# Kernel tuning notes

Hardware: AMD Instinct MI355X
Metric: run time of the kernel (lower is better)

The kernel has to match this reference:

```python
import jax, jax.numpy as jnp
import numpy as np

B, S, D, H, HD = 2, 2048, 1024, 16, 64
DFF = 4 * D
EPS = 1e-6


def _rms(x, w):
    return w * (x * jax.lax.rsqrt(jnp.mean(x * x, axis=-1, keepdims=True) + EPS))


def _rope(x, rope):
    # x: [B, H, S, HD], rope: [S, HD, 2]
    cos = rope[..., 0][None, None]
    sin = rope[..., 1][None, None]
    xr = x.reshape(*x.shape[:-1], -1, 2)
    rot = jnp.stack([-xr[..., 1], xr[..., 0]], axis=-1).reshape(x.shape)
    return x * cos + rot * sin


def setup_inputs() -> dict:
    key = jax.random.key(0)
    ks = jax.random.split(key, 10)
    w = lambda k, shape: jax.random.normal(k, shape, jnp.float32) * 0.02
    return {
        "hidden_states": jax.random.normal(ks[0], (B, S, D), jnp.float32),
        "timestep": jax.random.normal(ks[1], (B, D), jnp.float32),
        "rope_pos_embed": jax.random.normal(ks[2], (S, HD, 2), jnp.float32),
        "adaln_w": w(ks[3], (6 * D, D)),
        "adaln_b": jnp.zeros((6 * D,), jnp.float32),
        "wq": w(ks[4], (D, D)),
        "wk": w(ks[5], (D, D)),
        "wv": w(ks[6], (D, D)),
        "wo": w(ks[7], (D, D)),
        "q_norm_w": jnp.ones((D,), jnp.float32),
        "k_norm_w": jnp.ones((D,), jnp.float32),
        "norm3_w": jnp.ones((D,), jnp.float32),
        "fc1_w": w(ks[8], (DFF, D)),
        "fc1_b": jnp.zeros((DFF,), jnp.float32),
        "fc2_w": w(ks[9], (D, DFF)),
        "fc2_b": jnp.zeros((D,), jnp.float32),
    }


def reference(hidden_states, timestep, rope_pos_embed, adaln_w, adaln_b,
              wq, wk, wv, wo, q_norm_w, k_norm_w, norm3_w,
              fc1_w, fc1_b, fc2_w, fc2_b):
    x = hidden_states  # [B, S, D]
    # AdaLayerNorm: emb = Linear(SiLU(timestep)) -> 6 modulation chunks, broadcast over seq
    emb = jax.nn.silu(timestep) @ adaln_w.T + adaln_b  # [B, 6D]
    sh_msa, sc_msa, g_msa, sh_mlp, sc_mlp, g_mlp = jnp.split(emb[:, None, :], 6, axis=-1)
    mu = jnp.mean(x, axis=-1, keepdims=True)
    var = jnp.mean((x - mu) ** 2, axis=-1, keepdims=True)
    ln = (x - mu) * jax.lax.rsqrt(var + EPS)
    xm = ln * (1.0 + sc_msa) + sh_msa  # modulated input to attention

    # Attention: projections + RMSNorm over inner_dim + RoPE + SDPA
    q = _rms(xm @ wq.T, q_norm_w)
    k = _rms(xm @ wk.T, k_norm_w)
    v = xm @ wv.T
    q = q.reshape(B, S, H, HD).transpose(0, 2, 1, 3)
    k = k.reshape(B, S, H, HD).transpose(0, 2, 1, 3)
    v = v.reshape(B, S, H, HD).transpose(0, 2, 1, 3)
    q = _rope(q, rope_pos_embed)
    k = _rope(k, rope_pos_embed)
    scores = jnp.einsum('bhqd,bhkd->bhqk', q, k) * (HD ** -0.5)
    attn = jax.nn.softmax(scores, axis=-1)
    o = jnp.einsum('bhqk,bhkd->bhqd', attn, v)
    o = o.transpose(0, 2, 1, 3).reshape(B, S, H * HD) @ wo.T

    h = x + g_msa * o  # gated residual

    # MLP branch with AdaLN scale/shift on RMSNorm output
    n3 = _rms(h, norm3_w)
    nm = n3 * (1.0 + sc_mlp) + sh_mlp
    ff = jax.nn.gelu(nm @ fc1_w.T + fc1_b, approximate=True) @ fc2_w.T + fc2_b
    return h + g_mlp * ff
```

## Files before the change

### kernel.cpp

```cpp
#include <hip/hip_runtime.h>
#include <cstdint>
#include <cstddef>

typedef unsigned short ushort_t;
typedef __attribute__((ext_vector_type(8))) short s8v;
typedef __attribute__((ext_vector_type(4))) short s4v;
typedef __attribute__((ext_vector_type(4))) float f4v;

#define MFMA16(a, b, c) __builtin_amdgcn_mfma_f32_16x16x32_bf16(a, b, c, 0, 0, 0)

__device__ __forceinline__ ushort_t f2bf(float f) {
  union { float f; unsigned u; } a; a.f = f;
  return (ushort_t)((a.u + 0x7fffu + ((a.u >> 16) & 1u)) >> 16);
}
__device__ __forceinline__ float bf2f(ushort_t h) {
  union { unsigned u; float f; } a; a.u = ((unsigned)h) << 16; return a.f;
}
__device__ __forceinline__ unsigned fbits(float f) {
  union { float f; unsigned u; } a; a.f = f; return a.u;
}

__device__ __forceinline__ void gload16(const void* g, void* l) {
  __builtin_amdgcn_global_load_lds(
      (__attribute__((address_space(1))) void*)(uintptr_t)g,
      (__attribute__((address_space(3))) void*)(unsigned)(uintptr_t)l,
      16, 0, 0);
}

__launch_bounds__(256)
__global__ void convert_w(const float* __restrict__ wq, const float* __restrict__ wk,
                          const float* __restrict__ wv, const float* __restrict__ wo,
                          const float* __restrict__ f1, const float* __restrict__ f2,
                          ushort_t* __restrict__ dqkv, ushort_t* __restrict__ dwo,
                          ushort_t* __restrict__ df1, ushort_t* __restrict__ df2)
{
  const int blk = blockIdx.x;
  const float* src; ushort_t* dst; int off;
  if      (blk < 1024) { src = wq; dst = dqkv;            off = blk; }
  else if (blk < 2048) { src = wk; dst = dqkv + 1048576;  off = blk - 1024; }
  else if (blk < 3072) { src = wv; dst = dqkv + 2097152;  off = blk - 2048; }
  else if (blk < 4096) { src = wo; dst = dwo;             off = blk - 3072; }
  else if (blk < 8192) { src = f1; dst = df1;             off = blk - 4096; }
  else                 { src = f2; dst = df2;             off = blk - 8192; }
  const int idx = off * 1024 + threadIdx.x * 4;
  float4 v = *(const float4*)(src + idx);
  s4v o;
  o[0] = (short)f2bf(v.x); o[1] = (short)f2bf(v.y);
  o[2] = (short)f2bf(v.z); o[3] = (short)f2bf(v.w);
  *(s4v*)(dst + idx) = o;
}

__launch_bounds__(256)
__global__ void adaln(const float* __restrict__ ts, const float* __restrict__ w,
                      const float* __restrict__ bias, float* __restrict__ emb)
{
  const int j = blockIdx.x * 4 + (threadIdx.x >> 6);
  const int lane = threadIdx.x & 63;
  const float* wr = w + (size_t)j * 1024;
  float s0 = 0.f, s1 = 0.f;
  for (int i = lane; i < 1024; i += 64) {
    const float wv = wr[i];
    const float t0 = ts[i], t1 = ts[1024 + i];
    const float e0 = __builtin_amdgcn_exp2f(-1.4426950409f * t0);
    const float e1 = __builtin_amdgcn_exp2f(-1.4426950409f * t1);
    s0 += wv * t0 * __builtin_amdgcn_rcpf(1.f + e0);
    s1 += wv * t1 * __builtin_amdgcn_rcpf(1.f + e1);
  }
  #pragma unroll
  for (int m = 32; m; m >>= 1) { s0 += __shfl_down(s0, m); s1 += __shfl_down(s1, m); }
  if (!lane) { emb[j] = s0 + bias[j]; emb[6144 + j] = s1 + bias[j]; }
}

__launch_bounds__(256)
__global__ void ln_mod(const float* __restrict__ x, const float* __restrict__ emb,
                       ushort_t* __restrict__ xm)
{
  const int row = blockIdx.x, b = row >> 11, tid = threadIdx.x;
  const float* xr = x + (size_t)row * 1024;
  const int c = tid * 4;
  float4 v = *(const float4*)(xr + c);
  float s  = v.x + v.y + v.z + v.w;
  float s2 = v.x*v.x + v.y*v.y + v.z*v.z + v.w*v.w;
  #pragma unroll
  for (int m = 32; m; m >>= 1) { s += __shfl_down(s, m); s2 += __shfl_down(s2, m); }
  __shared__ float red[8];
  const int wave = tid >> 6, lane = tid & 63;
  if (!lane) { red[wave] = s; red[4 + wave] = s2; }
  __syncthreads();
  const float mu = (red[0] + red[1] + red[2] + red[3]) * (1.f / 1024.f);
  const float ms = (red[4] + red[5] + red[6] + red[7]) * (1.f / 1024.f);
  const float rstd = rsqrtf(ms - mu * mu + 1e-6f);
  const float* sh = emb + b * 6144;
  const float* sc = emb + b * 6144 + 1024;
  float4 shv = *(const float4*)(sh + c);
  float4 scv = *(const float4*)(sc + c);
  s4v ov;
  ov[0] = (short)f2bf((v.x - mu) * rstd * (1.f + scv.x) + shv.x);
  ov[1] = (short)f2bf((v.y - mu) * rstd * (1.f + scv.y) + shv.y);
  ov[2] = (short)f2bf((v.z - mu) * rstd * (1.f + scv.z) + shv.z);
  ov[3] = (short)f2bf((v.w - mu) * rstd * (1.f + scv.w) + shv.w);
  *(s4v*)(xm + (size_t)row * 1024 + c) = ov;
}

template<int EPI, int TN>
__launch_bounds__(256)
__global__ void gemm_bt(const ushort_t* __restrict__ A, const ushort_t* __restrict__ Bw,
                        int K, int N,
                        ushort_t* __restrict__ outb, float* __restrict__ outf,
                        const float* __restrict__ bias, const float* __restrict__ resid,
                        const float* __restrict__ emb, int gate_off)
{
  constexpr int JN = TN / 32;
  constexpr int BUFB = TN * 32;
  __shared__ ushort_t As0[128 * 32], As1[128 * 32];
  __shared__ ushort_t Bs0[BUFB],    Bs1[BUFB];
  const int tid = threadIdx.x;
  const int wave = tid >> 6, lane = tid & 63;
  const int quad = lane >> 4, r = lane & 15;
  const int m0 = blockIdx.y * 128, n0 = blockIdx.x * TN;
  const int wm = (wave >> 1) * 64, wn = (wave & 1) * (TN / 2);

  const int srow = wave * 16 + (lane >> 2);
  const int scol = (lane & 3) * 8;
  const ushort_t* ag = A  + (size_t)(m0 + srow) * K + scol;
  const ushort_t* bg = Bw + (size_t)(n0 + srow) * K + scol;
  const size_t rowK64 = (size_t)64 * K;

  f4v acc[4][JN] = {};

  auto stage = [&](ushort_t* as, ushort_t* bs) {
    gload16(ag,          as + wave * 512);
    gload16(ag + rowK64, as + wave * 512 + 2048);
    gload16(bg,          bs + wave * 512);
    if (TN == 128) gload16(bg + rowK64, bs + wave * 512 + 2048);
    ag += 32; bg += 32;
  };
  auto compute = [&](const ushort_t* ab, const ushort_t* bb) {
    s8v af[4], bf[JN];
    #pragma unroll
    for (int i = 0; i < 4; i++)
      af[i] = *(const s8v*)(ab + (wm + i * 16 + r) * 32 + quad * 8);
    #pragma unroll
    for (int j = 0; j < JN; j++)
      bf[j] = *(const s8v*)(bb + (wn + j * 16 + r) * 32 + quad * 8);
    #pragma unroll
    for (int i = 0; i < 4; i++)
      #pragma unroll
      for (int j = 0; j < JN; j++)
        acc[i][j] = MFMA16(af[i], bf[j], acc[i][j]);
  };

  stage(As0, Bs0);
  __syncthreads();
  const int R = (K >> 6) - 1;
  for (int it = 0; it < R; it++) {
    stage(As1, Bs1);
    compute(As0, Bs0);
    __syncthreads();
    stage(As0, Bs0);
    compute(As1, Bs1);
    __syncthreads();
  }
  stage(As1, Bs1);
  compute(As0, Bs0);
  __syncthreads();
  compute(As1, Bs1);

  const int bblk = m0 >> 11;
  #pragma unroll
  for (int j = 0; j < JN; j++) {
    const int col = n0 + wn + j * 16 + r;
    float bj = 0.f, gj = 0.f;
    if (EPI == 2 || EPI == 3) bj = bias[col];
    if (EPI == 1 || EPI == 3) gj = emb[bblk * 6144 + gate_off + col];
    #pragma unroll
    for (int i = 0; i < 4; i++) {
      const int row = m0 + wm + i * 16 + quad * 4;
      #pragma unroll
      for (int rr = 0; rr < 4; rr++) {
        float v = acc[i][j][rr];
        const size_t idx = (size_t)(row + rr) * N + col;
        if (EPI == 0) {
          outb[idx] = f2bf(v);
        } else if (EPI == 1) {
          outf[idx] = resid[idx] + gj * v;
        } else if (EPI == 2) {
          v += bj;
          const float t = fmaf(v * v, 0.1029436f, 2.3022083f);
          const float e = __builtin_amdgcn_exp2f(-v * t);
          outb[idx] = f2bf(v * __builtin_amdgcn_rcpf(1.f + e));
        } else {
          outf[idx] = resid[idx] + gj * (v + bj);
        }
      }
    }
  }
}

__launch_bounds__(256, 2)
__global__ void gemm256(const ushort_t* __restrict__ A, const ushort_t* __restrict__ Bw,
                        int K, int N,
                        ushort_t* __restrict__ outb, const float* __restrict__ bias)
{
  __shared__ ushort_t As0[256 * 32], As1[256 * 32];
  __shared__ ushort_t Bs0[128 * 32], Bs1[128 * 32];
  const int tid = threadIdx.x;
  const int wave = tid >> 6, lane = tid & 63;
  const int quad = lane >> 4, r = lane & 15;
  const int m0 = blockIdx.y * 256, n0 = blockIdx.x * 128;
  const int wm = (wave >> 1) * 128, wn = (wave & 1) * 64;

  const int srow = wave * 16 + (lane >> 2);
  const int scol = (lane & 3) * 8;
  const ushort_t* ag = A  + (size_t)(m0 + srow) * K + scol;
  const ushort_t* bg = Bw + (size_t)(n0 + srow) * K + scol;
  const size_t rowK64 = (size_t)64 * K;

  f4v acc[8][4] = {};

  auto stage = [&](ushort_t* as, ushort_t* bs) {
    #pragma unroll
    for (int sg = 0; sg < 4; sg++)
      gload16(ag + sg * rowK64, as + sg * 2048 + wave * 512);
    #pragma unroll
    for (int sg = 0; sg < 2; sg++)
      gload16(bg + sg * rowK64, bs + sg * 2048 + wave * 512);
    ag += 32; bg += 32;
  };
  auto compute = [&](const ushort_t* ab, const ushort_t* bb) {
    s8v bf[4];
    #pragma unroll
    for (int j = 0; j < 4; j++)
      bf[j] = *(const s8v*)(bb + (wn + j * 16 + r) * 32 + quad * 8);
    #pragma unroll
    for (int i = 0; i < 8; i++) {
      s8v af = *(const s8v*)(ab + (wm + i * 16 + r) * 32 + quad * 8);
      #pragma unroll
      for (int j = 0; j < 4; j++)
        acc[i][j] = MFMA16(af, bf[j], acc[i][j]);
    }
  };

  stage(As0, Bs0);
  __syncthreads();
  const int R = (K >> 6) - 1;
  for (int it = 0; it < R; it++) {
    stage(As1, Bs1);
    compute(As0, Bs0);
    __syncthreads();
    stage(As0, Bs0);
    compute(As1, Bs1);
    __syncthreads();
  }
  stage(As1, Bs1);
  compute(As0, Bs0);
  __syncthreads();
  compute(As1, Bs1);

  #pragma unroll
  for (int j = 0; j < 4; j++) {
    const int col = n0 + wn + j * 16 + r;
    const float bj = bias[col];
    #pragma unroll
    for (int i = 0; i < 8; i++) {
      const int row = m0 + wm + i * 16 + quad * 4;
      #pragma unroll
      for (int rr = 0; rr < 4; rr++) {
        float v = acc[i][j][rr] + bj;
        const float t = fmaf(v * v, 0.1029436f, 2.3022083f);
        const float e = __builtin_amdgcn_exp2f(-v * t);
        outb[(size_t)(row + rr) * N + col] =
            f2bf(v * __builtin_amdgcn_rcpf(1.f + e));
      }
    }
  }
}

__launch_bounds__(256)
__global__ void qkv_post(const ushort_t* __restrict__ qkv, const float* __restrict__ rope,
                         const float* __restrict__ qw, const float* __restrict__ kw,
                         ushort_t* __restrict__ q_r, ushort_t* __restrict__ k_r,
                         ushort_t* __restrict__ v_r)
{
  const int row = blockIdx.x, b = row >> 11, s = row & 2047, tid = threadIdx.x;
  const ushort_t* base = qkv + (size_t)row * 3072;
  const int c = tid * 4;
  s4v qv = *(const s4v*)(base + c);
  s4v kv = *(const s4v*)(base + 1024 + c);
  s4v vv = *(const s4v*)(base + 2048 + c);
  float qf[4], kf[4]; float sq = 0.f, sk = 0.f;
  #pragma unroll
  for (int i = 0; i < 4; i++) {
    qf[i] = bf2f((ushort_t)qv[i]); kf[i] = bf2f((ushort_t)kv[i]);
    sq += qf[i] * qf[i]; sk += kf[i] * kf[i];
  }
  #pragma unroll
  for (int m = 32; m; m >>= 1) { sq += __shfl_down(sq, m); sk += __shfl_down(sk, m); }
  __shared__ float red[8];
  const int wave = tid >> 6, lane = tid & 63;
  if (!lane) { red[wave] = sq; red[4 + wave] = sk; }
  __syncthreads();
  const float rq = rsqrtf((red[0]+red[1]+red[2]+red[3]) * (1.f/1024.f) + 1e-6f)
                   * 0.18033688011112042f;
  const float rk = rsqrtf((red[4]+red[5]+red[6]+red[7]) * (1.f/1024.f) + 1e-6f);

  const int h = c >> 6, d = c & 63;
  const float* rp = rope + ((size_t)s * 64 + d) * 2;
  float4 r01 = *(const float4*)(rp);
  float4 r23 = *(const float4*)(rp + 4);
  const float q0 = qf[0]*rq*qw[c], q1 = qf[1]*rq*qw[c+1];
  const float q2 = qf[2]*rq*qw[c+2], q3 = qf[3]*rq*qw[c+3];
  const float k0 = kf[0]*rk*kw[c], k1 = kf[1]*rk*kw[c+1];
  const float k2 = kf[2]*rk*kw[c+2], k3 = kf[3]*rk*kw[c+3];
  s4v qo, ko;
  qo[0] = (short)f2bf(q0 * r01.x - q1 * r01.y);
  qo[1] = (short)f2bf(q1 * r01.z + q0 * r01.w);
  qo[2] = (short)f2bf(q2 * r23.x - q3 * r23.y);
  qo[3] = (short)f2bf(q3 * r23.z + q2 * r23.w);
  ko[0] = (short)f2bf(k0 * r01.x - k1 * r01.y);
  ko[1] = (short)f2bf(k1 * r01.z + k0 * r01.w);
  ko[2] = (short)f2bf(k2 * r23.x - k3 * r23.y);
  ko[3] = (short)f2bf(k3 * r23.z + k2 * r23.w);
  const size_t rowbase = ((size_t)(b * 16 + h) * 2048 + s) * 64;
  const int d_s = (((d >> 3) ^ (s & 7)) << 3) | (d & 7);
  *(s4v*)(q_r + rowbase + d) = qo;
  *(s4v*)(k_r + rowbase + d_s) = ko;
  *(s4v*)(v_r + rowbase + d) = vv;
}

__launch_bounds__(256)
__global__ void vtrans(const ushort_t* __restrict__ v_r, ushort_t* __restrict__ v_t)
{
  const int bh = blockIdx.x >> 5, st = blockIdx.x & 31;
  const int s0 = st * 64;
  __shared__ ushort_t tile[64 * 72];
  const int tid = threadIdx.x;
  #pragma unroll
  for (int rep = 0; rep < 2; rep++) {
    const int idx = rep * 256 + tid;
    const int sr = idx >> 3, dc = (idx & 7) << 3;
    s8v val = *(const s8v*)(v_r + ((size_t)bh * 2048 + s0 + sr) * 64 + dc);
    *(s8v*)(tile + sr * 72 + dc) = val;
  }
  __syncthreads();
  #pragma unroll
  for (int rep = 0; rep < 2; rep++) {
    const int idx = rep * 256 + tid;
    const int d = idx >> 3;
    const int scs = (((idx & 7) ^ (d & 7)) << 3);
    s8v val;
    const int sc = (idx & 7) << 3;
    #pragma unroll
    for (int j = 0; j < 8; j++) val[j] = (short)tile[(sc + j) * 72 + d];
    *(s8v*)(v_t + ((size_t)bh * 64 + d) * 2048 + s0 + scs) = val;
  }
}

__launch_bounds__(256)
__global__ void flash(const ushort_t* __restrict__ q_r, const ushort_t* __restrict__ k_r,
                      const ushort_t* __restrict__ v_t, ushort_t* __restrict__ attn)
{
  __shared__ ushort_t Ksh[128 * 64];
  __shared__ ushort_t Vsh[64 * 128];
  __shared__ ushort_t Psh[4][16 * 128];
  const int bh = blockIdx.x >> 5, qb = blockIdx.x & 31;
  const int tid = threadIdx.x, wave = tid >> 6, lane = tid & 63;
  const int quad = lane >> 4, r = lane & 15;
  const int rx = r & 7;
  const int q0 = qb * 64 + wave * 16;
  const size_t bhS = (size_t)bh * 2048;

  s8v aq0 = *(const s8v*)(q_r + (bhS + q0 + r) * 64 + quad * 8);
  s8v aq1 = *(const s8v*)(q_r + (bhS + q0 + r) * 64 + 32 + quad * 8);

  f4v o[4] = {};
  float mi = -1e30f, li = 0.f;

  const ushort_t* kg = k_r + (bhS + wave * 32 + (lane >> 3)) * 64 + (lane & 7) * 8;
  ushort_t* kl = Ksh + wave * 2048 + lane * 8;
  const ushort_t* vg = v_t + ((size_t)bh * 64 + wave * 16 + (lane >> 4)) * 2048
                       + (lane & 15) * 8;
  ushort_t* vl = Vsh + (wave * 16 + (lane >> 4)) * 128 + (lane & 15) * 8;
  ushort_t* pw = &Psh[wave][0];

  for (int kb = 0; kb < 2048; kb += 128) {
    __syncthreads();
    #pragma unroll
    for (int c = 0; c < 4; c++) {
      gload16(kg + (size_t)(kb + c * 8) * 64, kl + c * 512);
      gload16(vg + kb + (size_t)(c * 4) * 2048, vl + c * 512);
    }
    __syncthreads();

    f4v st[8];
    #pragma unroll
    for (int t = 0; t < 8; t++) {
      const ushort_t* krow = Ksh + (t * 16 + r) * 64;
      s8v k0 = *(const s8v*)(krow + ((quad ^ rx) << 3));
      s8v k1 = *(const s8v*)(krow + (((4 + quad) ^ rx) << 3));
      f4v z = {};
      z = MFMA16(k0, aq0, z);
      z = MFMA16(k1, aq1, z);
      st[t] = z;
    }

    float m4[8];
    #pragma unroll
    for (int t = 0; t < 8; t++)
      m4[t] = fmaxf(fmaxf(st[t][0], st[t][1]), fmaxf(st[t][2], st[t][3]));
    float mloc = fmaxf(fmaxf(fmaxf(m4[0], m4[1]), fmaxf(m4[2], m4[3])),
                       fmaxf(fmaxf(m4[4], m4[5]), fmaxf(m4[6], m4[7])));
    mloc = fmaxf(mloc, __shfl_xor(mloc, 16));
    mloc = fmaxf(mloc, __shfl_xor(mloc, 32));
    const float mn = fmaxf(mi, mloc);
    const float al = __builtin_amdgcn_exp2f(mi - mn);

    float p[8][4];
    uint2 pk[8];
    #pragma unroll
    for (int t = 0; t < 8; t++) {
      #pragma unroll
      for (int rr = 0; rr < 4; rr++)
        p[t][rr] = __builtin_amdgcn_exp2f(st[t][rr] - mn);
      const unsigned u0 = fbits(p[t][0]) + 0x8000u;
      const unsigned u1 = fbits(p[t][1]) + 0x8000u;
      const unsigned u2 = fbits(p[t][2]) + 0x8000u;
      const unsigned u3 = fbits(p[t][3]) + 0x8000u;
      pk[t].x = __builtin_amdgcn_perm(u1, u0, 0x07060302u);
      pk[t].y = __builtin_amdgcn_perm(u3, u2, 0x07060302u);
    }

    #pragma unroll
    for (int t = 0; t < 8; t++) {
      const int cw = t * 2 + (quad >> 1);
      const int sc = (cw & 8) | ((cw & 7) ^ rx);
      *(uint2*)(pw + r * 128 + (sc << 3) + (quad & 1) * 4) = pk[t];
    }

    float alo[4];
    #pragma unroll
    for (int rr = 0; rr < 4; rr++) alo[rr] = __shfl(al, quad * 4 + rr);
    #pragma unroll
    for (int nt = 0; nt < 4; nt++)
      #pragma unroll
      for (int rr = 0; rr < 4; rr++) o[nt][rr] *= alo[rr];

    float s4r[8];
    #pragma unroll
    for (int t = 0; t < 8; t++)
      s4r[t] = (p[t][0] + p[t][1]) + (p[t][2] + p[t][3]);
    float ls = ((s4r[0] + s4r[1]) + (s4r[2] + s4r[3])) +
               ((s4r[4] + s4r[5]) + (s4r[6] + s4r[7]));
    ls += __shfl_xor(ls, 16);
    ls += __shfl_xor(ls, 32);
    li = al * li + ls;
    mi = mn;

    asm volatile("s_waitcnt lgkmcnt(0)" ::: "memory");

    #pragma unroll
    for (int kc = 0; kc < 4; kc++) {
      const int c = kc * 4 + quad;
      const int sc = (c & 8) | ((c & 7) ^ rx);
      s8v ap = *(const s8v*)(pw + r * 128 + (sc << 3));
      #pragma unroll
      for (int nt = 0; nt < 4; nt++) {
        s8v bv = *(const s8v*)(Vsh + (nt * 16 + r) * 128 + (sc << 3));
        o[nt] = MFMA16(ap, bv, o[nt]);
      }
    }
  }

  const int h = bh & 15, b = bh >> 4;
  const float linv = 1.f / li;
  #pragma unroll
  for (int rr = 0; rr < 4; rr++) {
    const float inv = __shfl(linv, quad * 4 + rr);
    const size_t orow = ((size_t)(b * 2048 + q0 + quad * 4 + rr)) * 1024 + h * 64;
    #pragma unroll
    for (int nt = 0; nt < 4; nt++)
      attn[orow + nt * 16 + r] = f2bf(o[nt][rr] * inv);
  }
}

__launch_bounds__(256)
__global__ void rms3_mod(const float* __restrict__ h, const float* __restrict__ emb,
                         const float* __restrict__ w3, ushort_t* __restrict__ nm)
{
  const int row = blockIdx.x, b = row >> 11, tid = threadIdx.x;
  const float* hr = h + (size_t)row * 1024;
  const int c = tid * 4;
  float4 v = *(const float4*)(hr + c);
  float s2 = v.x*v.x + v.y*v.y + v.z*v.z + v.w*v.w;
  #pragma unroll
  for (int m = 32; m; m >>= 1) s2 += __shfl_down(s2, m);
  __shared__ float red[4];
  const int wave = tid >> 6, lane = tid & 63;
  if (!lane) red[wave] = s2;
  __syncthreads();
  const float rms = rsqrtf((red[0] + red[1] + red[2] + red[3]) * (1.f / 1024.f) + 1e-6f);
  const float* sh = emb + b * 6144 + 3072;
  const float* sc = emb + b * 6144 + 4096;
  float4 shv = *(const float4*)(sh + c);
  float4 scv = *(const float4*)(sc + c);
  float4 wv  = *(const float4*)(w3 + c);
  s4v ov;
  ov[0] = (short)f2bf(v.x * rms * wv.x * (1.f + scv.x) + shv.x);
  ov[1] = (short)f2bf(v.y * rms * wv.y * (1.f + scv.y) + shv.y);
  ov[2] = (short)f2bf(v.z * rms * wv.z * (1.f + scv.z) + shv.z);
  ov[3] = (short)f2bf(v.w * rms * wv.w * (1.f + scv.w) + shv.w);
  *(s4v*)(nm + (size_t)row * 1024 + c) = ov;
}

extern "C" void kernel_launch(void* const* d_in, const int* in_sizes, int n_in,
                              void* d_out, int out_size, void* d_ws, size_t ws_size,
                              hipStream_t stream)
{
  const float* x    = (const float*)d_in[0];
  const float* ts   = (const float*)d_in[1];
  const float* rope = (const float*)d_in[2];
  const float* adw  = (const float*)d_in[3];
  const float* adb  = (const float*)d_in[4];
  const float* wq   = (const float*)d_in[5];
  const float* wk   = (const float*)d_in[6];
  const float* wv   = (const float*)d_in[7];
  const float* wo   = (const float*)d_in[8];
  const float* qnw  = (const float*)d_in[9];
  const float* knw  = (const float*)d_in[10];
  const float* n3w  = (const float*)d_in[11];
  const float* f1w  = (const float*)d_in[12];
  const float* f1b  = (const float*)d_in[13];
  const float* f2w  = (const float*)d_in[14];
  const float* f2b  = (const float*)d_in[15];

  char* ws = (char*)d_ws;
  ushort_t* WQKV = (ushort_t*)(ws + 0);
  ushort_t* WO   = (ushort_t*)(ws + 6291456);
  ushort_t* F1   = (ushort_t*)(ws + 8388608);
  ushort_t* F2   = (ushort_t*)(ws + 16777216);
  float*    EMB  = (float*)   (ws + 25165824);
  float*    H    = (float*)   (ws + 25214976);
  ushort_t* XM   = (ushort_t*)(ws + 41992192);
  ushort_t* QKV  = (ushort_t*)(ws + 50380800);
  ushort_t* QR   = (ushort_t*)(ws + 75546624);
  ushort_t* KR   = (ushort_t*)(ws + 83935232);
  ushort_t* VR   = (ushort_t*)(ws + 92323840);
  ushort_t* VT   = (ushort_t*)(ws + 100712448);
  ushort_t* ATTN = XM;
  ushort_t* NM   = QKV;
  ushort_t* FF1  = QR;

  convert_w<<<12288, 256, 0, stream>>>(wq, wk, wv, wo, f1w, f2w, WQKV, WO, F1, F2);
  adaln<<<1536, 256, 0, stream>>>(ts, adw, adb, EMB);
  ln_mod<<<4096, 256, 0, stream>>>(x, EMB, XM);
  gemm_bt<0, 128><<<dim3(24, 32), 256, 0, stream>>>(XM, WQKV, 1024, 3072,
      QKV, nullptr, nullptr, nullptr, nullptr, 0);
  qkv_post<<<4096, 256, 0, stream>>>(QKV, rope, qnw, knw, QR, KR, VR);
  vtrans<<<1024, 256, 0, stream>>>(VR, VT);
  flash<<<1024, 256, 0, stream>>>(QR, KR, VT, ATTN);
  gemm_bt<1, 64><<<dim3(16, 32), 256, 0, stream>>>(ATTN, WO, 1024, 1024,
      nullptr, H, nullptr, x, EMB, 2048);
  rms3_mod<<<4096, 256, 0, stream>>>(H, EMB, n3w, NM);
  gemm256<<<dim3(32, 16), 256, 0, stream>>>(NM, F1, 1024, 4096, FF1, f1b);
  gemm_bt<3, 64><<<dim3(16, 32), 256, 0, stream>>>(FF1, F2, 4096, 1024,
      nullptr, (float*)d_out, f2b, H, EMB, 5120);
}
```

Measured before the change: 425.7 us.

## Double-buffer K/V tiles in flash attention and raise wave priority around MFMAs

The flash attention kernel now keeps two LDS buffers for K and V. It issues the global-to-LDS loads for the next 128-key tile while the current tile is being computed, replacing the load, barrier, compute sequence with a ping-pong pipeline. It also wraps the QK and PV MFMA loops in s_setprio to favour matrix issue. The aim is to hide global load latency behind compute. In exchange, LDS per block grows from about 48KB to 80KB, which may lower occupancy.

Result: faster. 414.7 us (-2.6%).

```diff
diff --git a/kernel.cpp b/kernel.cpp
--- a/kernel.cpp
+++ b/kernel.cpp
@@ -360,8 +360,8 @@
 __global__ void flash(const ushort_t* __restrict__ q_r, const ushort_t* __restrict__ k_r,
                       const ushort_t* __restrict__ v_t, ushort_t* __restrict__ attn)
 {
-  __shared__ ushort_t Ksh[128 * 64];
-  __shared__ ushort_t Vsh[64 * 128];
+  __shared__ ushort_t Ksh[2][128 * 64];
+  __shared__ ushort_t Vsh[2][64 * 128];
   __shared__ ushort_t Psh[4][16 * 128];
   const int bh = blockIdx.x >> 5, qb = blockIdx.x & 31;
   const int tid = threadIdx.x, wave = tid >> 6, lane = tid & 63;
@@ -377,25 +377,26 @@
   float mi = -1e30f, li = 0.f;
 
   const ushort_t* kg = k_r + (bhS + wave * 32 + (lane >> 3)) * 64 + (lane & 7) * 8;
-  ushort_t* kl = Ksh + wave * 2048 + lane * 8;
   const ushort_t* vg = v_t + ((size_t)bh * 64 + wave * 16 + (lane >> 4)) * 2048
                        + (lane & 15) * 8;
-  ushort_t* vl = Vsh + (wave * 16 + (lane >> 4)) * 128 + (lane & 15) * 8;
+  const int klo = wave * 2048 + lane * 8;
+  const int vlo = (wave * 16 + (lane >> 4)) * 128 + (lane & 15) * 8;
   ushort_t* pw = &Psh[wave][0];
 
-  for (int kb = 0; kb < 2048; kb += 128) {
-    __syncthreads();
+  auto stage = [&](ushort_t* kbuf, ushort_t* vbuf, int kb) {
     #pragma unroll
     for (int c = 0; c < 4; c++) {
-      gload16(kg + (size_t)(kb + c * 8) * 64, kl + c * 512);
-      gload16(vg + kb + (size_t)(c * 4) * 2048, vl + c * 512);
-    }
-    __syncthreads();
-
+      gload16(kg + (size_t)(kb + c * 8) * 64, kbuf + klo + c * 512);
+      gload16(vg + kb + (size_t)(c * 4) * 2048, vbuf + vlo + c * 512);
+    }
+  };
+
+  auto step = [&](const ushort_t* Kc, const ushort_t* Vc) {
     f4v st[8];
+    __builtin_amdgcn_s_setprio(1);
     #pragma unroll
     for (int t = 0; t < 8; t++) {
-      const ushort_t* krow = Ksh + (t * 16 + r) * 64;
+      const ushort_t* krow = Kc + (t * 16 + r) * 64;
       s8v k0 = *(const s8v*)(krow + ((quad ^ rx) << 3));
       s8v k1 = *(const s8v*)(krow + (((4 + quad) ^ rx) << 3));
       f4v z = {};
@@ -403,6 +404,7 @@
       z = MFMA16(k1, aq1, z);
       st[t] = z;
     }
+    __builtin_amdgcn_s_setprio(0);
 
     float m4[8];
     #pragma unroll
@@ -458,6 +460,7 @@
 
     asm volatile("s_waitcnt lgkmcnt(0)" ::: "memory");
 
+    __builtin_amdgcn_s_setprio(1);
     #pragma unroll
     for (int kc = 0; kc < 4; kc++) {
       const int c = kc * 4 + quad;
@@ -465,10 +468,24 @@
       s8v ap = *(const s8v*)(pw + r * 128 + (sc << 3));
       #pragma unroll
       for (int nt = 0; nt < 4; nt++) {
-        s8v bv = *(const s8v*)(Vsh + (nt * 16 + r) * 128 + (sc << 3));
+        s8v bv = *(const s8v*)(Vc + (nt * 16 + r) * 128 + (sc << 3));
         o[nt] = MFMA16(ap, bv, o[nt]);
       }
     }
+    __builtin_amdgcn_s_setprio(0);
+  };
+
+  stage(Ksh[0], Vsh[0], 0);
+  __syncthreads();
+
+  #pragma unroll 1
+  for (int kb = 0; kb < 2048; kb += 256) {
+    stage(Ksh[1], Vsh[1], kb + 128);
+    step(Ksh[0], Vsh[0]);
+    __syncthreads();
+    if (kb + 256 < 2048) stage(Ksh[0], Vsh[0], kb + 256);
+    step(Ksh[1], Vsh[1]);
+    __syncthreads();
   }
 
   const int h = bh & 15, b = bh >> 4;
```
